# Kernel optimization log

Hardware: AMD Instinct MI355X
Metric: run time of the kernel (lower is better)

The kernel has to match this reference:

```python
import jax, jax.numpy as jnp
import numpy as np

DIM = 512
HEADS = 8
DIM_HEAD = 64
INNER = HEADS * DIM_HEAD
SCALE = DIM_HEAD ** -0.5


def setup_inputs() -> dict:
    key = jax.random.key(0)
    ks = jax.random.split(key, 6)
    b, n = 2, 2048
    x = jax.random.normal(ks[0], (b, n, DIM), dtype=jnp.float32)
    # torch Linear(dim, 3*inner, bias=False): store as [in, out] for x @ W
    w_qkv = jax.random.normal(ks[1], (DIM, 3 * INNER), dtype=jnp.float32) * (DIM ** -0.5)
    # Conv2d(heads, heads, 1, bias=False) weights squeezed to [out_h, in_h]
    w_pre = jax.random.normal(ks[2], (HEADS, HEADS), dtype=jnp.float32) * (HEADS ** -0.5)
    w_post = jax.random.normal(ks[3], (HEADS, HEADS), dtype=jnp.float32) * (HEADS ** -0.5)
    w_out = jax.random.normal(ks[4], (INNER, DIM), dtype=jnp.float32) * (INNER ** -0.5)
    b_out = jax.random.normal(ks[5], (DIM,), dtype=jnp.float32) * 0.01
    return {"x": x, "w_qkv": w_qkv, "w_pre": w_pre, "w_post": w_post,
            "w_out": w_out, "b_out": b_out}


def reference(x, w_qkv, w_pre, w_post, w_out, b_out):
    b, n, _ = x.shape
    qkv = x @ w_qkv  # [b, n, 3*inner]
    q, k, v = jnp.split(qkv, 3, axis=-1)
    # b n (h d) -> b h n d
    split_heads = lambda t: t.reshape(b, n, HEADS, DIM_HEAD).transpose(0, 2, 1, 3)
    q, k, v = split_heads(q), split_heads(k), split_heads(v)
    dots = jnp.einsum('bhid,bhjd->bhij', q, k) * SCALE
    # pre-softmax talking-heads: 1x1 conv over the head axis
    dots = jnp.einsum('gh,bhij->bgij', w_pre, dots)
    attn = jax.nn.softmax(dots, axis=-1)
    # post-softmax talking-heads mix
    attn = jnp.einsum('gh,bhij->bgij', w_post, attn)
    out = jnp.einsum('bhij,bhjd->bhid', attn, v)
    out = out.transpose(0, 2, 1, 3).reshape(b, n, INNER)  # b h n d -> b n (h d)
    return out @ w_out + b_out
```

## Files before the change

kernel.cpp:

```cpp
#include <hip/hip_runtime.h>
#include <hip/hip_bf16.h>

typedef unsigned short ushort_t;
typedef __attribute__((ext_vector_type(8))) short short8;
typedef __attribute__((ext_vector_type(4))) short short4v;
typedef __attribute__((ext_vector_type(4))) float floatx4;

#define MFMA16(a, b, c) __builtin_amdgcn_mfma_f32_16x16x32_bf16(a, b, c, 0, 0, 0)

__device__ __forceinline__ float bf2f(ushort_t u) {
    unsigned int v = ((unsigned int)u) << 16;
    return __int_as_float((int)v);
}
__device__ __forceinline__ ushort_t f2bf(float f) {
    unsigned int x = (unsigned int)__float_as_int(f);
    unsigned int r = (x + 0x7FFFu + ((x >> 16) & 1u)) >> 16;
    return (ushort_t)r;
}

__global__ __launch_bounds__(256) void k_cvt(const floatx4* __restrict__ src,
                                             short4v* __restrict__ dst, int n4) {
    int i = blockIdx.x * 256 + threadIdx.x;
    if (i < n4) {
        floatx4 v = src[i];
        short4v o;
        o[0] = (short)f2bf(v[0]);
        o[1] = (short)f2bf(v[1]);
        o[2] = (short)f2bf(v[2]);
        o[3] = (short)f2bf(v[3]);
        dst[i] = o;
    }
}

__global__ __launch_bounds__(256) void k_transpose_cvt(const float* __restrict__ src,
                                                       ushort_t* __restrict__ dst, int R, int C) {
    __shared__ float t[32][33];
    int tx = threadIdx.x & 31, ty = threadIdx.x >> 5;
    int r0 = blockIdx.y * 32, c0 = blockIdx.x * 32;
    for (int y = ty; y < 32; y += 8) t[y][tx] = src[(r0 + y) * C + c0 + tx];
    __syncthreads();
    for (int y = ty; y < 32; y += 8) dst[(c0 + y) * R + r0 + tx] = f2bf(t[tx][y]);
}

__global__ __launch_bounds__(256) void k_qkv(const ushort_t* __restrict__ x,
                                             const ushort_t* __restrict__ wt,
                                             ushort_t* __restrict__ qs,
                                             ushort_t* __restrict__ ks,
                                             ushort_t* __restrict__ vt) {
    __shared__ __align__(16) ushort_t st[64 * 72];
    const int tid = threadIdx.x, lane = tid & 63, wv = tid >> 6;
    const int col = lane & 15, quad = lane >> 4;
    const int row0 = blockIdx.y * 64 + (wv >> 1) * 32;
    const int c0 = blockIdx.x * 64 + (wv & 1) * 32;
    const int which = blockIdx.x >> 3, hh = blockIdx.x & 7;
    const int brow0 = blockIdx.y * 64;
    const int bb = brow0 >> 11, n0 = brow0 & 2047;
    const int hidx = bb * 8 + hh;
    floatx4 acc[2][2];
#pragma unroll
    for (int i = 0; i < 2; i++)
#pragma unroll
        for (int j = 0; j < 2; j++) acc[i][j] = (floatx4){0.f, 0.f, 0.f, 0.f};
    for (int k0 = 0; k0 < 512; k0 += 32) {
        const int ko = k0 + quad * 8;
        short8 a0 = *(const short8*)&x[(row0 + col) * 512 + ko];
        short8 a1 = *(const short8*)&x[(row0 + 16 + col) * 512 + ko];
        short8 b0 = *(const short8*)&wt[(c0 + col) * 512 + ko];
        short8 b1 = *(const short8*)&wt[(c0 + 16 + col) * 512 + ko];
        acc[0][0] = MFMA16(a0, b0, acc[0][0]);
        acc[0][1] = MFMA16(a0, b1, acc[0][1]);
        acc[1][0] = MFMA16(a1, b0, acc[1][0]);
        acc[1][1] = MFMA16(a1, b1, acc[1][1]);
    }
    const float qscale = (which == 0) ? 0.125f : 1.0f;
#pragma unroll
    for (int i = 0; i < 2; i++)
#pragma unroll
        for (int j = 0; j < 2; j++)
#pragma unroll
            for (int r = 0; r < 4; r++) {
                int il = (wv >> 1) * 32 + i * 16 + quad * 4 + r;
                int cl = (wv & 1) * 32 + j * 16 + col;
                ushort_t hv = f2bf(acc[i][j][r] * qscale);
                if (which == 2) st[cl * 72 + il] = hv;
                else            st[il * 72 + cl] = hv;
            }
    __syncthreads();
    if (which < 2) {
        ushort_t* dst = (which == 0) ? qs : ks;
#pragma unroll
        for (int s = tid; s < 512; s += 256) {
            int rr = s >> 3, dc = (s & 7) * 8;
            *(short8*)&dst[(hidx * 2048 + n0 + rr) * 64 + dc] = *(const short8*)&st[rr * 72 + dc];
        }
    } else {
#pragma unroll
        for (int s = tid; s < 512; s += 256) {
            int d = s >> 3, nc = (s & 7) * 8;
            *(short8*)&vt[(hidx * 64 + d) * 2048 + n0 + nc] = *(const short8*)&st[d * 72 + nc];
        }
    }
}

__global__ __launch_bounds__(256, 4) void k_stats(const ushort_t* __restrict__ qs,
                                                  const ushort_t* __restrict__ ks,
                                                  const float* __restrict__ w_pre,
                                                  float* __restrict__ lpart) {
    __shared__ __align__(16) ushort_t qlds[8 * 16 * 72];
    __shared__ float lred[4][8][16];
    const int tid = threadIdx.x, lane = tid & 63, wv = tid >> 6;
    const int col = lane & 15, quad = lane >> 4;
    const int jc = blockIdx.x, b = blockIdx.z, n0 = blockIdx.y * 16;
    for (int c = tid; c < 1024; c += 256) {
        int hh = c >> 7, rem = c & 127, ii = rem >> 3, dc = (rem & 7) * 8;
        *(short8*)&qlds[(hh * 16 + ii) * 72 + dc] =
            *(const short8*)&qs[((b * 8 + hh) * 2048 + n0 + ii) * 64 + dc];
    }
    __syncthreads();
    float Lacc[8][4];
#pragma unroll
    for (int g = 0; g < 8; g++)
#pragma unroll
        for (int r = 0; r < 4; r++) Lacc[g][r] = 0.f;
    for (int it = 0; it < 8; it++) {
        const int jw = jc * 512 + it * 64 + wv * 16;
        floatx4 S[8];
#pragma unroll
        for (int h = 0; h < 8; h++) {
            const ushort_t* qb = &qlds[(h * 16 + col) * 72 + quad * 8];
            short8 a0 = *(const short8*)&qb[0];
            short8 a1 = *(const short8*)&qb[32];
            const ushort_t* kb = &ks[((b * 8 + h) * 2048 + jw + col) * 64 + quad * 8];
            short8 b0 = *(const short8*)&kb[0];
            short8 b1 = *(const short8*)&kb[32];
            floatx4 a = (floatx4){0.f, 0.f, 0.f, 0.f};
            a = MFMA16(a0, b0, a);
            a = MFMA16(a1, b1, a);
            S[h] = a;
        }
#pragma unroll
        for (int g = 0; g < 8; g++)
#pragma unroll
            for (int r = 0; r < 4; r++) {
                float s = 0.f;
#pragma unroll
                for (int h = 0; h < 8; h++) s = fmaf(w_pre[g * 8 + h], S[h][r], s);
                Lacc[g][r] += __expf(s);
            }
    }
#pragma unroll
    for (int g = 0; g < 8; g++)
#pragma unroll
        for (int r = 0; r < 4; r++) {
            float v = Lacc[g][r];
            v += __shfl_xor(v, 1, 64);
            v += __shfl_xor(v, 2, 64);
            v += __shfl_xor(v, 4, 64);
            v += __shfl_xor(v, 8, 64);
            if (col == 0) lred[wv][g][quad * 4 + r] = v;
        }
    __syncthreads();
    if (tid < 128) {
        int g = tid >> 4, ii = tid & 15;
        float l = lred[0][g][ii] + lred[1][g][ii] + lred[2][g][ii] + lred[3][g][ii];
        lpart[((b * 4 + jc) * 8 + g) * 2048 + n0 + ii] = l;
    }
}

__global__ __launch_bounds__(512, 2) void k_attn(const ushort_t* __restrict__ qs,
                                                 const ushort_t* __restrict__ ks,
                                                 const ushort_t* __restrict__ vt,
                                                 const float* __restrict__ w_pre,
                                                 const float* __restrict__ w_post,
                                                 const float* __restrict__ lpart,
                                                 const ushort_t* __restrict__ wot,
                                                 const float* __restrict__ bias,
                                                 float* __restrict__ out) {
    __shared__ __align__(16) ushort_t qlds[8 * 16 * 72];
    __shared__ __align__(16) ushort_t amix[8 * 16 * 136];
    __shared__ __align__(16) ushort_t oline[16 * 520];
    __shared__ float linv[8][16];
    const int tid = threadIdx.x, lane = tid & 63, wv = tid >> 6;
    const int col = lane & 15, quad = lane >> 4;
    const int b = blockIdx.y, n0 = blockIdx.x * 16;
    const int e = wv;

    for (int c = tid; c < 1024; c += 512) {
        int hh = c >> 7, rem = c & 127, ii = rem >> 3, dc = (rem & 7) * 8;
        *(short8*)&qlds[(hh * 16 + ii) * 72 + dc] =
            *(const short8*)&qs[((b * 8 + hh) * 2048 + n0 + ii) * 64 + dc];
    }
    if (tid < 128) {
        int g = tid >> 4, ii = tid & 15;
        float l = 0.f;
#pragma unroll
        for (int jc = 0; jc < 4; jc++) l += lpart[((b * 4 + jc) * 8 + g) * 2048 + n0 + ii];
        linv[g][ii] = 1.0f / l;
    }
    __syncthreads();
    float lr[8][4];
#pragma unroll
    for (int g = 0; g < 8; g++)
#pragma unroll
        for (int r = 0; r < 4; r++) lr[g][r] = linv[g][quad * 4 + r];

    floatx4 O[4];
#pragma unroll
    for (int nt = 0; nt < 4; nt++) O[nt] = (floatx4){0.f, 0.f, 0.f, 0.f};

    for (int jt = 0; jt < 16; jt++) {
        const int j0 = jt * 128;
        const int jw = j0 + wv * 16;
        floatx4 S[8];
#pragma unroll
        for (int h = 0; h < 8; h++) {
            const ushort_t* qb = &qlds[(h * 16 + col) * 72 + quad * 8];
            short8 a0 = *(const short8*)&qb[0];
            short8 a1 = *(const short8*)&qb[32];
            const ushort_t* kb = &ks[((b * 8 + h) * 2048 + jw + col) * 64 + quad * 8];
            short8 b0 = *(const short8*)&kb[0];
            short8 b1 = *(const short8*)&kb[32];
            floatx4 a = (floatx4){0.f, 0.f, 0.f, 0.f};
            a = MFMA16(a0, b0, a);
            a = MFMA16(a1, b1, a);
            S[h] = a;
        }
        float P[8][4];
#pragma unroll
        for (int g = 0; g < 8; g++)
#pragma unroll
            for (int r = 0; r < 4; r++) {
                float s = 0.f;
#pragma unroll
                for (int h = 0; h < 8; h++) s = fmaf(w_pre[g * 8 + h], S[h][r], s);
                P[g][r] = __expf(s) * lr[g][r];
            }
#pragma unroll
        for (int e2 = 0; e2 < 8; e2++)
#pragma unroll
            for (int r = 0; r < 4; r++) {
                float a = 0.f;
#pragma unroll
                for (int g = 0; g < 8; g++) a = fmaf(w_post[e2 * 8 + g], P[g][r], a);
                amix[(e2 * 16 + quad * 4 + r) * 136 + wv * 16 + col] = f2bf(a);
            }
        __syncthreads();
#pragma unroll
        for (int nt = 0; nt < 4; nt++) {
            floatx4 a = O[nt];
#pragma unroll
            for (int k2 = 0; k2 < 4; k2++) {
                short8 af = *(const short8*)&amix[(e * 16 + col) * 136 + k2 * 32 + quad * 8];
                short8 bf = *(const short8*)&vt[((b * 8 + e) * 64 + nt * 16 + col) * 2048 + j0 +
                                                k2 * 32 + quad * 8];
                a = MFMA16(af, bf, a);
            }
            O[nt] = a;
        }
        __syncthreads();
    }
#pragma unroll
    for (int nt = 0; nt < 4; nt++)
#pragma unroll
        for (int r = 0; r < 4; r++)
            oline[(quad * 4 + r) * 520 + e * 64 + nt * 16 + col] = f2bf(O[nt][r]);
    __syncthreads();
#pragma unroll
    for (int nt = 0; nt < 4; nt++) {
        floatx4 acc = (floatx4){0.f, 0.f, 0.f, 0.f};
        const int c = wv * 64 + nt * 16 + col;
#pragma unroll
        for (int k2 = 0; k2 < 16; k2++) {
            short8 af = *(const short8*)&oline[col * 520 + k2 * 32 + quad * 8];
            short8 bf = *(const short8*)&wot[c * 512 + k2 * 32 + quad * 8];
            acc = MFMA16(af, bf, acc);
        }
        float bz = bias[c];
#pragma unroll
        for (int r = 0; r < 4; r++)
            out[(b * 2048 + n0 + quad * 4 + r) * 512 + c] = acc[r] + bz;
    }
}

extern "C" void kernel_launch(void* const* d_in, const int* in_sizes, int n_in,
                              void* d_out, int out_size, void* d_ws, size_t ws_size,
                              hipStream_t stream) {
    const float* x = (const float*)d_in[0];
    const float* w_qkv = (const float*)d_in[1];
    const float* w_pre = (const float*)d_in[2];
    const float* w_post = (const float*)d_in[3];
    const float* w_out = (const float*)d_in[4];
    const float* b_out = (const float*)d_in[5];
    char* ws = (char*)d_ws;
    ushort_t* qs = (ushort_t*)(ws);
    ushort_t* ks = (ushort_t*)(ws + (4u << 20));
    ushort_t* vt = (ushort_t*)(ws + (8u << 20));
    ushort_t* xb = (ushort_t*)(ws + (12u << 20));
    ushort_t* wt = (ushort_t*)(ws + (16u << 20));
    ushort_t* wot = (ushort_t*)(ws + (16u << 20) + 1572864u);
    float* lpart = (float*)(ws + (18u << 20));
    float* out = (float*)d_out;

    k_cvt<<<dim3(2048), dim3(256), 0, stream>>>((const floatx4*)x, (short4v*)xb, 524288);
    k_transpose_cvt<<<dim3(48, 16), dim3(256), 0, stream>>>(w_qkv, wt, 512, 1536);
    k_transpose_cvt<<<dim3(16, 16), dim3(256), 0, stream>>>(w_out, wot, 512, 512);
    k_qkv<<<dim3(24, 64), dim3(256), 0, stream>>>(xb, wt, qs, ks, vt);
    k_stats<<<dim3(4, 128, 2), dim3(256), 0, stream>>>(qs, ks, w_pre, lpart);
    k_attn<<<dim3(128, 2), dim3(512), 0, stream>>>(qs, ks, vt, w_pre, w_post, lpart, wot, b_out, out);
}
```

Baseline: 379.6 us.

## Split attention over key chunks with atomic output accumulation and retile QKV GEMM

```diff
diff --git a/kernel.cpp b/kernel.cpp
--- a/kernel.cpp
+++ b/kernel.cpp
@@ -5,6 +5,7 @@
 typedef __attribute__((ext_vector_type(8))) short short8;
 typedef __attribute__((ext_vector_type(4))) short short4v;
 typedef __attribute__((ext_vector_type(4))) float floatx4;
+typedef __attribute__((ext_vector_type(2))) float floatx2;
 
 #define MFMA16(a, b, c) __builtin_amdgcn_mfma_f32_16x16x32_bf16(a, b, c, 0, 0, 0)
 
@@ -42,62 +43,68 @@
     for (int y = ty; y < 32; y += 8) dst[(c0 + y) * R + r0 + tx] = f2bf(t[tx][y]);
 }
 
-__global__ __launch_bounds__(256) void k_qkv(const ushort_t* __restrict__ x,
-                                             const ushort_t* __restrict__ wt,
-                                             ushort_t* __restrict__ qs,
-                                             ushort_t* __restrict__ ks,
-                                             ushort_t* __restrict__ vt) {
-    __shared__ __align__(16) ushort_t st[64 * 72];
+__global__ __launch_bounds__(256, 3) void k_qkv(const ushort_t* __restrict__ x,
+                                                const ushort_t* __restrict__ wt,
+                                                ushort_t* __restrict__ qs,
+                                                ushort_t* __restrict__ ks,
+                                                ushort_t* __restrict__ vt) {
+    __shared__ __align__(16) ushort_t st[9216];
     const int tid = threadIdx.x, lane = tid & 63, wv = tid >> 6;
     const int col = lane & 15, quad = lane >> 4;
-    const int row0 = blockIdx.y * 64 + (wv >> 1) * 32;
-    const int c0 = blockIdx.x * 64 + (wv & 1) * 32;
     const int which = blockIdx.x >> 3, hh = blockIdx.x & 7;
-    const int brow0 = blockIdx.y * 64;
-    const int bb = brow0 >> 11, n0 = brow0 & 2047;
+    const int c0 = blockIdx.x * 64;
+    const int absrow0 = blockIdx.y * 128;
+    const int bb = blockIdx.y >> 4, n0 = (blockIdx.y & 15) * 128;
     const int hidx = bb * 8 + hh;
-    floatx4 acc[2][2];
+    const int row0 = absrow0 + wv * 32;
+    floatx4 acc[2][4];
 #pragma unroll
     for (int i = 0; i < 2; i++)
 #pragma unroll
-        for (int j = 0; j < 2; j++) acc[i][j] = (floatx4){0.f, 0.f, 0.f, 0.f};
+        for (int j = 0; j < 4; j++) acc[i][j] = (floatx4){0.f, 0.f, 0.f, 0.f};
     for (int k0 = 0; k0 < 512; k0 += 32) {
         const int ko = k0 + quad * 8;
         short8 a0 = *(const short8*)&x[(row0 + col) * 512 + ko];
         short8 a1 = *(const short8*)&x[(row0 + 16 + col) * 512 + ko];
         short8 b0 = *(const short8*)&wt[(c0 + col) * 512 + ko];
         short8 b1 = *(const short8*)&wt[(c0 + 16 + col) * 512 + ko];
+        short8 b2 = *(const short8*)&wt[(c0 + 32 + col) * 512 + ko];
+        short8 b3 = *(const short8*)&wt[(c0 + 48 + col) * 512 + ko];
         acc[0][0] = MFMA16(a0, b0, acc[0][0]);
         acc[0][1] = MFMA16(a0, b1, acc[0][1]);
+        acc[0][2] = MFMA16(a0, b2, acc[0][2]);
+        acc[0][3] = MFMA16(a0, b3, acc[0][3]);
         acc[1][0] = MFMA16(a1, b0, acc[1][0]);
         acc[1][1] = MFMA16(a1, b1, acc[1][1]);
+        acc[1][2] = MFMA16(a1, b2, acc[1][2]);
+        acc[1][3] = MFMA16(a1, b3, acc[1][3]);
     }
     const float qscale = (which == 0) ? 0.125f : 1.0f;
 #pragma unroll
     for (int i = 0; i < 2; i++)
 #pragma unroll
-        for (int j = 0; j < 2; j++)
+        for (int j = 0; j < 4; j++)
 #pragma unroll
             for (int r = 0; r < 4; r++) {
-                int il = (wv >> 1) * 32 + i * 16 + quad * 4 + r;
-                int cl = (wv & 1) * 32 + j * 16 + col;
+                int il = wv * 32 + i * 16 + quad * 4 + r;
+                int cl = j * 16 + col;
                 ushort_t hv = f2bf(acc[i][j][r] * qscale);
-                if (which == 2) st[cl * 72 + il] = hv;
+                if (which == 2) st[cl * 136 + il] = hv;
                 else            st[il * 72 + cl] = hv;
             }
     __syncthreads();
     if (which < 2) {
         ushort_t* dst = (which == 0) ? qs : ks;
 #pragma unroll
-        for (int s = tid; s < 512; s += 256) {
+        for (int s = tid; s < 1024; s += 256) {
             int rr = s >> 3, dc = (s & 7) * 8;
             *(short8*)&dst[(hidx * 2048 + n0 + rr) * 64 + dc] = *(const short8*)&st[rr * 72 + dc];
         }
     } else {
 #pragma unroll
-        for (int s = tid; s < 512; s += 256) {
-            int d = s >> 3, nc = (s & 7) * 8;
-            *(short8*)&vt[(hidx * 64 + d) * 2048 + n0 + nc] = *(const short8*)&st[d * 72 + nc];
+        for (int s = tid; s < 1024; s += 256) {
+            int d = s >> 4, nc = (s & 15) * 8;
+            *(short8*)&vt[(hidx * 64 + d) * 2048 + n0 + nc] = *(const short8*)&st[d * 136 + nc];
         }
     }
 }
@@ -117,11 +124,11 @@
             *(const short8*)&qs[((b * 8 + hh) * 2048 + n0 + ii) * 64 + dc];
     }
     __syncthreads();
-    float Lacc[8][4];
+    floatx2 Lacc[8][2];
 #pragma unroll
     for (int g = 0; g < 8; g++)
 #pragma unroll
-        for (int r = 0; r < 4; r++) Lacc[g][r] = 0.f;
+        for (int r2 = 0; r2 < 2; r2++) Lacc[g][r2] = (floatx2){0.f, 0.f};
     for (int it = 0; it < 8; it++) {
         const int jw = jc * 512 + it * 64 + wv * 16;
         floatx4 S[8];
@@ -141,18 +148,21 @@
 #pragma unroll
         for (int g = 0; g < 8; g++)
 #pragma unroll
-            for (int r = 0; r < 4; r++) {
-                float s = 0.f;
-#pragma unroll
-                for (int h = 0; h < 8; h++) s = fmaf(w_pre[g * 8 + h], S[h][r], s);
-                Lacc[g][r] += __expf(s);
+            for (int r2 = 0; r2 < 2; r2++) {
+                floatx2 s = (floatx2){0.f, 0.f};
+#pragma unroll
+                for (int h = 0; h < 8; h++) {
+                    floatx2 sv = (floatx2){S[h][2 * r2], S[h][2 * r2 + 1]};
+                    s += sv * w_pre[g * 8 + h];
+                }
+                Lacc[g][r2] += (floatx2){__expf(s.x), __expf(s.y)};
             }
     }
 #pragma unroll
     for (int g = 0; g < 8; g++)
 #pragma unroll
         for (int r = 0; r < 4; r++) {
-            float v = Lacc[g][r];
+            float v = (r & 1) ? Lacc[g][r >> 1].y : Lacc[g][r >> 1].x;
             v += __shfl_xor(v, 1, 64);
             v += __shfl_xor(v, 2, 64);
             v += __shfl_xor(v, 4, 64);
@@ -167,7 +177,7 @@
     }
 }
 
-__global__ __launch_bounds__(512, 2) void k_attn(const ushort_t* __restrict__ qs,
+__global__ __launch_bounds__(512, 4) void k_attn(const ushort_t* __restrict__ qs,
                                                  const ushort_t* __restrict__ ks,
                                                  const ushort_t* __restrict__ vt,
                                                  const float* __restrict__ w_pre,
@@ -178,11 +188,10 @@
                                                  float* __restrict__ out) {
     __shared__ __align__(16) ushort_t qlds[8 * 16 * 72];
     __shared__ __align__(16) ushort_t amix[8 * 16 * 136];
-    __shared__ __align__(16) ushort_t oline[16 * 520];
     __shared__ float linv[8][16];
     const int tid = threadIdx.x, lane = tid & 63, wv = tid >> 6;
     const int col = lane & 15, quad = lane >> 4;
-    const int b = blockIdx.y, n0 = blockIdx.x * 16;
+    const int jc = blockIdx.x, b = blockIdx.z, n0 = blockIdx.y * 16;
     const int e = wv;
 
     for (int c = tid; c < 1024; c += 512) {
@@ -194,7 +203,7 @@
         int g = tid >> 4, ii = tid & 15;
         float l = 0.f;
 #pragma unroll
-        for (int jc = 0; jc < 4; jc++) l += lpart[((b * 4 + jc) * 8 + g) * 2048 + n0 + ii];
+        for (int q2 = 0; q2 < 4; q2++) l += lpart[((b * 4 + q2) * 8 + g) * 2048 + n0 + ii];
         linv[g][ii] = 1.0f / l;
     }
     __syncthreads();
@@ -208,8 +217,8 @@
 #pragma unroll
     for (int nt = 0; nt < 4; nt++) O[nt] = (floatx4){0.f, 0.f, 0.f, 0.f};
 
-    for (int jt = 0; jt < 16; jt++) {
-        const int j0 = jt * 128;
+    for (int tl = 0; tl < 4; tl++) {
+        const int j0 = jc * 512 + tl * 128;
         const int jw = j0 + wv * 16;
         floatx4 S[8];
 #pragma unroll
@@ -225,24 +234,28 @@
             a = MFMA16(a1, b1, a);
             S[h] = a;
         }
-        float P[8][4];
+        floatx2 P[8][2];
 #pragma unroll
         for (int g = 0; g < 8; g++)
 #pragma unroll
-            for (int r = 0; r < 4; r++) {
-                float s = 0.f;
-#pragma unroll
-                for (int h = 0; h < 8; h++) s = fmaf(w_pre[g * 8 + h], S[h][r], s);
-                P[g][r] = __expf(s) * lr[g][r];
+            for (int r2 = 0; r2 < 2; r2++) {
+                floatx2 s = (floatx2){0.f, 0.f};
+#pragma unroll
+                for (int h = 0; h < 8; h++) {
+                    floatx2 sv = (floatx2){S[h][2 * r2], S[h][2 * r2 + 1]};
+                    s += sv * w_pre[g * 8 + h];
+                }
+                P[g][r2] = (floatx2){__expf(s.x) * lr[g][2 * r2], __expf(s.y) * lr[g][2 * r2 + 1]};
             }
 #pragma unroll
         for (int e2 = 0; e2 < 8; e2++)
 #pragma unroll
-            for (int r = 0; r < 4; r++) {
-                float a = 0.f;
-#pragma unroll
-                for (int g = 0; g < 8; g++) a = fmaf(w_post[e2 * 8 + g], P[g][r], a);
-                amix[(e2 * 16 + quad * 4 + r) * 136 + wv * 16 + col] = f2bf(a);
+            for (int r2 = 0; r2 < 2; r2++) {
+                floatx2 a = (floatx2){0.f, 0.f};
+#pragma unroll
+                for (int g = 0; g < 8; g++) a += P[g][r2] * w_post[e2 * 8 + g];
+                amix[(e2 * 16 + quad * 4 + 2 * r2) * 136 + wv * 16 + col] = f2bf(a.x);
+                amix[(e2 * 16 + quad * 4 + 2 * r2 + 1) * 136 + wv * 16 + col] = f2bf(a.y);
             }
         __syncthreads();
 #pragma unroll
@@ -259,6 +272,7 @@
         }
         __syncthreads();
     }
+    ushort_t* oline = amix;
 #pragma unroll
     for (int nt = 0; nt < 4; nt++)
 #pragma unroll
@@ -275,10 +289,10 @@
             short8 bf = *(const short8*)&wot[c * 512 + k2 * 32 + quad * 8];
             acc = MFMA16(af, bf, acc);
         }
-        float bz = bias[c];
+        float bz = (jc == 0) ? bias[c] : 0.0f;
 #pragma unroll
         for (int r = 0; r < 4; r++)
-            out[(b * 2048 + n0 + quad * 4 + r) * 512 + c] = acc[r] + bz;
+            atomicAdd(&out[(b * 2048 + n0 + quad * 4 + r) * 512 + c], acc[r] + bz);
     }
 }
 
@@ -301,10 +315,12 @@
     float* lpart = (float*)(ws + (18u << 20));
     float* out = (float*)d_out;
 
+    hipMemsetAsync(d_out, 0, (size_t)out_size * sizeof(float), stream);
     k_cvt<<<dim3(2048), dim3(256), 0, stream>>>((const floatx4*)x, (short4v*)xb, 524288);
     k_transpose_cvt<<<dim3(48, 16), dim3(256), 0, stream>>>(w_qkv, wt, 512, 1536);
     k_transpose_cvt<<<dim3(16, 16), dim3(256), 0, stream>>>(w_out, wot, 512, 512);
-    k_qkv<<<dim3(24, 64), dim3(256), 0, stream>>>(xb, wt, qs, ks, vt);
+    k_qkv<<<dim3(24, 32), dim3(256), 0, stream>>>(xb, wt, qs, ks, vt);
     k_stats<<<dim3(4, 128, 2), dim3(256), 0, stream>>>(qs, ks, w_pre, lpart);
-    k_attn<<<dim3(128, 2), dim3(512), 0, stream>>>(qs, ks, vt, w_pre, w_post, lpart, wot, b_out, out);
-}
+    k_attn<<<dim3(4, 128, 2), dim3(512), 0, stream>>>(qs, ks, vt, w_pre, w_post, lpart, wot,
+                                                      b_out, out);
+}
```

After: 374.3 us. No clear change (-1.4%).

## Fuse softmax stats pass into attention kernel and enlarge QKV and PV tiles

Applied to the files above, without the earlier changes.

```diff
diff --git a/kernel.cpp b/kernel.cpp
--- a/kernel.cpp
+++ b/kernel.cpp
@@ -5,6 +5,7 @@
 typedef __attribute__((ext_vector_type(8))) short short8;
 typedef __attribute__((ext_vector_type(4))) short short4v;
 typedef __attribute__((ext_vector_type(4))) float floatx4;
+typedef __attribute__((ext_vector_type(2))) float floatx2;
 
 #define MFMA16(a, b, c) __builtin_amdgcn_mfma_f32_16x16x32_bf16(a, b, c, 0, 0, 0)
 
@@ -42,88 +43,103 @@
     for (int y = ty; y < 32; y += 8) dst[(c0 + y) * R + r0 + tx] = f2bf(t[tx][y]);
 }
 
-__global__ __launch_bounds__(256) void k_qkv(const ushort_t* __restrict__ x,
-                                             const ushort_t* __restrict__ wt,
-                                             ushort_t* __restrict__ qs,
-                                             ushort_t* __restrict__ ks,
-                                             ushort_t* __restrict__ vt) {
-    __shared__ __align__(16) ushort_t st[64 * 72];
+__global__ __launch_bounds__(256, 3) void k_qkv(const ushort_t* __restrict__ x,
+                                                const ushort_t* __restrict__ wt,
+                                                ushort_t* __restrict__ qs,
+                                                ushort_t* __restrict__ ks,
+                                                ushort_t* __restrict__ vt) {
+    __shared__ __align__(16) ushort_t st[9216];
     const int tid = threadIdx.x, lane = tid & 63, wv = tid >> 6;
     const int col = lane & 15, quad = lane >> 4;
-    const int row0 = blockIdx.y * 64 + (wv >> 1) * 32;
-    const int c0 = blockIdx.x * 64 + (wv & 1) * 32;
     const int which = blockIdx.x >> 3, hh = blockIdx.x & 7;
-    const int brow0 = blockIdx.y * 64;
-    const int bb = brow0 >> 11, n0 = brow0 & 2047;
+    const int c0 = blockIdx.x * 64;
+    const int absrow0 = blockIdx.y * 128;
+    const int bb = blockIdx.y >> 4, n0 = (blockIdx.y & 15) * 128;
     const int hidx = bb * 8 + hh;
-    floatx4 acc[2][2];
+    const int row0 = absrow0 + wv * 32;
+    floatx4 acc[2][4];
 #pragma unroll
     for (int i = 0; i < 2; i++)
 #pragma unroll
-        for (int j = 0; j < 2; j++) acc[i][j] = (floatx4){0.f, 0.f, 0.f, 0.f};
+        for (int j = 0; j < 4; j++) acc[i][j] = (floatx4){0.f, 0.f, 0.f, 0.f};
     for (int k0 = 0; k0 < 512; k0 += 32) {
         const int ko = k0 + quad * 8;
         short8 a0 = *(const short8*)&x[(row0 + col) * 512 + ko];
         short8 a1 = *(const short8*)&x[(row0 + 16 + col) * 512 + ko];
         short8 b0 = *(const short8*)&wt[(c0 + col) * 512 + ko];
         short8 b1 = *(const short8*)&wt[(c0 + 16 + col) * 512 + ko];
+        short8 b2 = *(const short8*)&wt[(c0 + 32 + col) * 512 + ko];
+        short8 b3 = *(const short8*)&wt[(c0 + 48 + col) * 512 + ko];
         acc[0][0] = MFMA16(a0, b0, acc[0][0]);
         acc[0][1] = MFMA16(a0, b1, acc[0][1]);
+        acc[0][2] = MFMA16(a0, b2, acc[0][2]);
+        acc[0][3] = MFMA16(a0, b3, acc[0][3]);
         acc[1][0] = MFMA16(a1, b0, acc[1][0]);
         acc[1][1] = MFMA16(a1, b1, acc[1][1]);
+        acc[1][2] = MFMA16(a1, b2, acc[1][2]);
+        acc[1][3] = MFMA16(a1, b3, acc[1][3]);
     }
     const float qscale = (which == 0) ? 0.125f : 1.0f;
 #pragma unroll
     for (int i = 0; i < 2; i++)
 #pragma unroll
-        for (int j = 0; j < 2; j++)
+        for (int j = 0; j < 4; j++)
 #pragma unroll
             for (int r = 0; r < 4; r++) {
-                int il = (wv >> 1) * 32 + i * 16 + quad * 4 + r;
-                int cl = (wv & 1) * 32 + j * 16 + col;
+                int il = wv * 32 + i * 16 + quad * 4 + r;
+                int cl = j * 16 + col;
                 ushort_t hv = f2bf(acc[i][j][r] * qscale);
-                if (which == 2) st[cl * 72 + il] = hv;
+                if (which == 2) st[cl * 136 + il] = hv;
                 else            st[il * 72 + cl] = hv;
             }
     __syncthreads();
     if (which < 2) {
         ushort_t* dst = (which == 0) ? qs : ks;
 #pragma unroll
-        for (int s = tid; s < 512; s += 256) {
+        for (int s = tid; s < 1024; s += 256) {
             int rr = s >> 3, dc = (s & 7) * 8;
             *(short8*)&dst[(hidx * 2048 + n0 + rr) * 64 + dc] = *(const short8*)&st[rr * 72 + dc];
         }
     } else {
 #pragma unroll
-        for (int s = tid; s < 512; s += 256) {
-            int d = s >> 3, nc = (s & 7) * 8;
-            *(short8*)&vt[(hidx * 64 + d) * 2048 + n0 + nc] = *(const short8*)&st[d * 72 + nc];
-        }
-    }
-}
-
-__global__ __launch_bounds__(256, 4) void k_stats(const ushort_t* __restrict__ qs,
-                                                  const ushort_t* __restrict__ ks,
-                                                  const float* __restrict__ w_pre,
-                                                  float* __restrict__ lpart) {
+        for (int s = tid; s < 1024; s += 256) {
+            int d = s >> 4, nc = (s & 15) * 8;
+            *(short8*)&vt[(hidx * 64 + d) * 2048 + n0 + nc] = *(const short8*)&st[d * 136 + nc];
+        }
+    }
+}
+
+__global__ __launch_bounds__(512, 2) void k_attn(const ushort_t* __restrict__ qs,
+                                                 const ushort_t* __restrict__ ks,
+                                                 const ushort_t* __restrict__ vt,
+                                                 const float* __restrict__ w_pre,
+                                                 const float* __restrict__ w_post,
+                                                 const ushort_t* __restrict__ wot,
+                                                 const float* __restrict__ bias,
+                                                 float* __restrict__ out) {
     __shared__ __align__(16) ushort_t qlds[8 * 16 * 72];
-    __shared__ float lred[4][8][16];
+    __shared__ __align__(16) ushort_t amix[8 * 16 * 264];
+    __shared__ float lred[8][8][16];
+    __shared__ float linv[8][16];
     const int tid = threadIdx.x, lane = tid & 63, wv = tid >> 6;
     const int col = lane & 15, quad = lane >> 4;
-    const int jc = blockIdx.x, b = blockIdx.z, n0 = blockIdx.y * 16;
-    for (int c = tid; c < 1024; c += 256) {
+    const int b = blockIdx.y, n0 = blockIdx.x * 16;
+    const int e = wv;
+
+    for (int c = tid; c < 1024; c += 512) {
         int hh = c >> 7, rem = c & 127, ii = rem >> 3, dc = (rem & 7) * 8;
         *(short8*)&qlds[(hh * 16 + ii) * 72 + dc] =
             *(const short8*)&qs[((b * 8 + hh) * 2048 + n0 + ii) * 64 + dc];
     }
     __syncthreads();
+
     float Lacc[8][4];
 #pragma unroll
     for (int g = 0; g < 8; g++)
 #pragma unroll
         for (int r = 0; r < 4; r++) Lacc[g][r] = 0.f;
-    for (int it = 0; it < 8; it++) {
-        const int jw = jc * 512 + it * 64 + wv * 16;
+    for (int t = 0; t < 16; t++) {
+        const int jw = wv * 256 + t * 16;
         floatx4 S[8];
 #pragma unroll
         for (int h = 0; h < 8; h++) {
@@ -162,39 +178,9 @@
     __syncthreads();
     if (tid < 128) {
         int g = tid >> 4, ii = tid & 15;
-        float l = lred[0][g][ii] + lred[1][g][ii] + lred[2][g][ii] + lred[3][g][ii];
-        lpart[((b * 4 + jc) * 8 + g) * 2048 + n0 + ii] = l;
-    }
-}
-
-__global__ __launch_bounds__(512, 2) void k_attn(const ushort_t* __restrict__ qs,
-                                                 const ushort_t* __restrict__ ks,
-                                                 const ushort_t* __restrict__ vt,
-                                                 const float* __restrict__ w_pre,
-                                                 const float* __restrict__ w_post,
-                                                 const float* __restrict__ lpart,
-                                                 const ushort_t* __restrict__ wot,
-                                                 const float* __restrict__ bias,
-                                                 float* __restrict__ out) {
-    __shared__ __align__(16) ushort_t qlds[8 * 16 * 72];
-    __shared__ __align__(16) ushort_t amix[8 * 16 * 136];
-    __shared__ __align__(16) ushort_t oline[16 * 520];
-    __shared__ float linv[8][16];
-    const int tid = threadIdx.x, lane = tid & 63, wv = tid >> 6;
-    const int col = lane & 15, quad = lane >> 4;
-    const int b = blockIdx.y, n0 = blockIdx.x * 16;
-    const int e = wv;
-
-    for (int c = tid; c < 1024; c += 512) {
-        int hh = c >> 7, rem = c & 127, ii = rem >> 3, dc = (rem & 7) * 8;
-        *(short8*)&qlds[(hh * 16 + ii) * 72 + dc] =
-            *(const short8*)&qs[((b * 8 + hh) * 2048 + n0 + ii) * 64 + dc];
-    }
-    if (tid < 128) {
-        int g = tid >> 4, ii = tid & 15;
         float l = 0.f;
 #pragma unroll
-        for (int jc = 0; jc < 4; jc++) l += lpart[((b * 4 + jc) * 8 + g) * 2048 + n0 + ii];
+        for (int w2 = 0; w2 < 8; w2++) l += lred[w2][g][ii];
         linv[g][ii] = 1.0f / l;
     }
     __syncthreads();
@@ -208,57 +194,59 @@
 #pragma unroll
     for (int nt = 0; nt < 4; nt++) O[nt] = (floatx4){0.f, 0.f, 0.f, 0.f};
 
-    for (int jt = 0; jt < 16; jt++) {
-        const int j0 = jt * 128;
-        const int jw = j0 + wv * 16;
-        floatx4 S[8];
-#pragma unroll
-        for (int h = 0; h < 8; h++) {
-            const ushort_t* qb = &qlds[(h * 16 + col) * 72 + quad * 8];
-            short8 a0 = *(const short8*)&qb[0];
-            short8 a1 = *(const short8*)&qb[32];
-            const ushort_t* kb = &ks[((b * 8 + h) * 2048 + jw + col) * 64 + quad * 8];
-            short8 b0 = *(const short8*)&kb[0];
-            short8 b1 = *(const short8*)&kb[32];
-            floatx4 a = (floatx4){0.f, 0.f, 0.f, 0.f};
-            a = MFMA16(a0, b0, a);
-            a = MFMA16(a1, b1, a);
-            S[h] = a;
-        }
-        float P[8][4];
-#pragma unroll
-        for (int g = 0; g < 8; g++)
-#pragma unroll
-            for (int r = 0; r < 4; r++) {
-                float s = 0.f;
-#pragma unroll
-                for (int h = 0; h < 8; h++) s = fmaf(w_pre[g * 8 + h], S[h][r], s);
-                P[g][r] = __expf(s) * lr[g][r];
-            }
-#pragma unroll
-        for (int e2 = 0; e2 < 8; e2++)
-#pragma unroll
-            for (int r = 0; r < 4; r++) {
-                float a = 0.f;
-#pragma unroll
-                for (int g = 0; g < 8; g++) a = fmaf(w_post[e2 * 8 + g], P[g][r], a);
-                amix[(e2 * 16 + quad * 4 + r) * 136 + wv * 16 + col] = f2bf(a);
-            }
+    for (int tile = 0; tile < 8; tile++) {
+        const int j0t = tile * 256;
+#pragma unroll
+        for (int sub = 0; sub < 2; sub++) {
+            const int jw = j0t + wv * 32 + sub * 16;
+            floatx4 S[8];
+#pragma unroll
+            for (int h = 0; h < 8; h++) {
+                const ushort_t* qb = &qlds[(h * 16 + col) * 72 + quad * 8];
+                short8 a0 = *(const short8*)&qb[0];
+                short8 a1 = *(const short8*)&qb[32];
+                const ushort_t* kb = &ks[((b * 8 + h) * 2048 + jw + col) * 64 + quad * 8];
+                short8 b0 = *(const short8*)&kb[0];
+                short8 b1 = *(const short8*)&kb[32];
+                floatx4 a = (floatx4){0.f, 0.f, 0.f, 0.f};
+                a = MFMA16(a0, b0, a);
+                a = MFMA16(a1, b1, a);
+                S[h] = a;
+            }
+            float P[8][4];
+#pragma unroll
+            for (int g = 0; g < 8; g++)
+#pragma unroll
+                for (int r = 0; r < 4; r++) {
+                    float s = 0.f;
+#pragma unroll
+                    for (int h = 0; h < 8; h++) s = fmaf(w_pre[g * 8 + h], S[h][r], s);
+                    P[g][r] = __expf(s) * lr[g][r];
+                }
+#pragma unroll
+            for (int e2 = 0; e2 < 8; e2++)
+#pragma unroll
+                for (int r = 0; r < 4; r++) {
+                    float a = 0.f;
+#pragma unroll
+                    for (int g = 0; g < 8; g++) a = fmaf(w_post[e2 * 8 + g], P[g][r], a);
+                    amix[(e2 * 16 + quad * 4 + r) * 264 + wv * 32 + sub * 16 + col] = f2bf(a);
+                }
+        }
         __syncthreads();
 #pragma unroll
-        for (int nt = 0; nt < 4; nt++) {
-            floatx4 a = O[nt];
-#pragma unroll
-            for (int k2 = 0; k2 < 4; k2++) {
-                short8 af = *(const short8*)&amix[(e * 16 + col) * 136 + k2 * 32 + quad * 8];
-                short8 bf = *(const short8*)&vt[((b * 8 + e) * 64 + nt * 16 + col) * 2048 + j0 +
+        for (int k2 = 0; k2 < 8; k2++) {
+            short8 af = *(const short8*)&amix[(e * 16 + col) * 264 + k2 * 32 + quad * 8];
+#pragma unroll
+            for (int nt = 0; nt < 4; nt++) {
+                short8 bf = *(const short8*)&vt[((b * 8 + e) * 64 + nt * 16 + col) * 2048 + j0t +
                                                 k2 * 32 + quad * 8];
-                a = MFMA16(af, bf, a);
-            }
-            O[nt] = a;
+                O[nt] = MFMA16(af, bf, O[nt]);
+            }
         }
         __syncthreads();
     }
+    ushort_t* oline = amix;
 #pragma unroll
     for (int nt = 0; nt < 4; nt++)
 #pragma unroll
@@ -298,13 +286,11 @@
     ushort_t* xb = (ushort_t*)(ws + (12u << 20));
     ushort_t* wt = (ushort_t*)(ws + (16u << 20));
     ushort_t* wot = (ushort_t*)(ws + (16u << 20) + 1572864u);
-    float* lpart = (float*)(ws + (18u << 20));
     float* out = (float*)d_out;
 
     k_cvt<<<dim3(2048), dim3(256), 0, stream>>>((const floatx4*)x, (short4v*)xb, 524288);
     k_transpose_cvt<<<dim3(48, 16), dim3(256), 0, stream>>>(w_qkv, wt, 512, 1536);
     k_transpose_cvt<<<dim3(16, 16), dim3(256), 0, stream>>>(w_out, wot, 512, 512);
-    k_qkv<<<dim3(24, 64), dim3(256), 0, stream>>>(xb, wt, qs, ks, vt);
-    k_stats<<<dim3(4, 128, 2), dim3(256), 0, stream>>>(qs, ks, w_pre, lpart);
-    k_attn<<<dim3(128, 2), dim3(512), 0, stream>>>(qs, ks, vt, w_pre, w_post, lpart, wot, b_out, out);
-}
+    k_qkv<<<dim3(24, 32), dim3(256), 0, stream>>>(xb, wt, qs, ks, vt);
+    k_attn<<<dim3(128, 2), dim3(512), 0, stream>>>(qs, ks, vt, w_pre, w_post, wot, b_out, out);
+}
```

After: 344.9 us. 9.1% less time.
